# Kernel tuning notes

Hardware: AMD Instinct MI355X
Metric: run time of the kernel (lower is better)

Reference implementation:

```python
import jax, jax.numpy as jnp
import numpy as np

VOCAB, DIM, HEADS, LAYERS = 32000, 1024, 16, 2
B, S = 2, 1024
HD = DIM // HEADS


def rmsnorm(x, g, eps=1e-6):
    return x * jax.lax.rsqrt(jnp.mean(x * x, axis=-1, keepdims=True) + eps) * g


def setup_inputs() -> dict:
    key = jax.random.key(0)
    ks = jax.random.split(key, 20)
    s = 0.02
    d = {
        "text_ids": jax.random.randint(ks[0], (B, S), 0, VOCAB),
        "embed": jax.random.normal(ks[1], (VOCAB, DIM), jnp.float32) * s,
        "g1": jnp.ones((LAYERS, DIM), jnp.float32),
        "wq": jax.random.normal(ks[2], (LAYERS, DIM, DIM), jnp.float32) * s,
        "bq": jnp.zeros((LAYERS, DIM), jnp.float32),
        "wk": jax.random.normal(ks[3], (LAYERS, DIM, DIM), jnp.float32) * s,
        "bk": jnp.zeros((LAYERS, DIM), jnp.float32),
        "wv": jax.random.normal(ks[4], (LAYERS, DIM, DIM), jnp.float32) * s,
        "bv": jnp.zeros((LAYERS, DIM), jnp.float32),
        "wo": jax.random.normal(ks[5], (LAYERS, DIM, DIM), jnp.float32) * s,
        "bo": jnp.zeros((LAYERS, DIM), jnp.float32),
        "g2": jnp.ones((LAYERS, DIM), jnp.float32),
        "w1": jax.random.normal(ks[6], (LAYERS, DIM, 4 * DIM), jnp.float32) * s,
        "b1": jnp.zeros((LAYERS, 4 * DIM), jnp.float32),
        "w2": jax.random.normal(ks[7], (LAYERS, 4 * DIM, DIM), jnp.float32) * s,
        "b2": jnp.zeros((LAYERS, DIM), jnp.float32),
        "gf": jnp.ones((DIM,), jnp.float32),
        "head_w": jax.random.normal(ks[8], (DIM, VOCAB), jnp.float32) * s,
        "head_b": jnp.zeros((VOCAB,), jnp.float32),
    }
    return d


def reference(text_ids, embed, g1, wq, bq, wk, bk, wv, bv, wo, bo,
              g2, w1, b1, w2, b2, gf, head_w, head_b):
    b, s = text_ids.shape
    x = embed[text_ids]                                   # [B,S,D]
    causal = jnp.tril(jnp.ones((s, s), dtype=bool))        # [S,S]
    scale = 1.0 / jnp.sqrt(jnp.asarray(HD, x.dtype))
    for l in range(LAYERS):
        # attention sublayer: x = x + attn(norm1(x))
        h = rmsnorm(x, g1[l])
        q = (h @ wq[l] + bq[l]).reshape(b, s, HEADS, HD)
        k = (h @ wk[l] + bk[l]).reshape(b, s, HEADS, HD)
        v = (h @ wv[l] + bv[l]).reshape(b, s, HEADS, HD)
        scores = jnp.einsum("bqhd,bkhd->bhqk", q, k) * scale
        scores = jnp.where(causal, scores, jnp.asarray(-1e30, scores.dtype))
        a = jax.nn.softmax(scores, axis=-1)
        o = jnp.einsum("bhqk,bkhd->bqhd", a, v).reshape(b, s, DIM)
        x = x + (o @ wo[l] + bo[l])
        # FFN sublayer: x = x + ffn(norm2(x)), SiLU MLP (MoE unused in source forward)
        h2 = rmsnorm(x, g2[l])
        x = x + (jax.nn.silu(h2 @ w1[l] + b1[l]) @ w2[l] + b2[l])
    x = rmsnorm(x, gf)
    return x.astype(jnp.float32) @ head_w + head_b         # [B,S,VOCAB]
```

## Files before the change

### kernel.cpp

```cpp
#include <hip/hip_runtime.h>

#define LAYERS 2
#define DIM 1024
#define HEADS 16
#define HD 64
#define BATCH 2
#define SEQ 1024
#define ROWS (BATCH * SEQ)
#define FFN (4 * DIM)
#define VOCAB 32000
#define QKVN (3 * DIM)

typedef unsigned short u16;
typedef short vshort8 __attribute__((ext_vector_type(8)));
typedef float f32x4 __attribute__((ext_vector_type(4)));

#define VMCNT(n) asm volatile("s_waitcnt vmcnt(" #n ")" ::: "memory")

__device__ __forceinline__ u16 f2bf(float f) {
  union { float f; unsigned u; } x{f};
  unsigned r = (x.u + 0x7fffu + ((x.u >> 16) & 1u)) >> 16;
  return (u16)r;
}

__device__ __forceinline__ void gll16(const void* g, u16* l) {
  __builtin_amdgcn_global_load_lds(
      (const __attribute__((address_space(1))) void*)g,
      (__attribute__((address_space(3))) void*)l, 16, 0, 0);
}

__device__ __forceinline__ int xcd_swizzle(int orig, int nwg) {
  int q = nwg >> 3, r = nwg & 7;
  int xcd = orig & 7;
  int base = (xcd < r) ? xcd * (q + 1) : r * (q + 1) + (xcd - r) * q;
  return base + (orig >> 3);
}

__global__ __launch_bounds__(256) void transpose_f32_bf16(
    const float* __restrict__ src, u16* __restrict__ dst, int R, int C) {
  __shared__ float tile[32][33];
  int c0 = blockIdx.x * 32, r0 = blockIdx.y * 32;
  int tx = threadIdx.x, ty = threadIdx.y;
#pragma unroll
  for (int i = 0; i < 4; i++)
    tile[ty + i * 8][tx] = src[(size_t)(r0 + ty + i * 8) * C + c0 + tx];
  __syncthreads();
#pragma unroll
  for (int i = 0; i < 4; i++)
    dst[(size_t)(c0 + ty + i * 8) * R + r0 + tx] = f2bf(tile[tx][ty + i * 8]);
}

__global__ __launch_bounds__(256) void pack_qkv_bias(
    const float* __restrict__ bq, const float* __restrict__ bk,
    const float* __restrict__ bv, float* __restrict__ o) {
  int t = blockIdx.x * 256 + threadIdx.x;
  if (t < DIM) o[t] = bq[t];
  else if (t < 2 * DIM) o[t] = bk[t - DIM];
  else if (t < 3 * DIM) o[t] = bv[t - 2 * DIM];
}

__global__ __launch_bounds__(256) void embed_gather(
    const int* __restrict__ ids, const float* __restrict__ emb,
    float* __restrict__ x) {
  int row = blockIdx.x;
  int id = ids[row];
  const float4* s = (const float4*)(emb + (size_t)id * DIM);
  float4* d = (float4*)(x + (size_t)row * DIM);
  d[threadIdx.x] = s[threadIdx.x];
}

__global__ __launch_bounds__(256) void rmsnorm_kernel(
    const float* __restrict__ x, const float* __restrict__ g,
    u16* __restrict__ out) {
  int row = blockIdx.x;
  int t = threadIdx.x;
  const float4* xr = (const float4*)(x + (size_t)row * DIM);
  float4 v = xr[t];
  float ss = v.x * v.x + v.y * v.y + v.z * v.z + v.w * v.w;
  for (int off = 32; off > 0; off >>= 1) ss += __shfl_down(ss, off);
  __shared__ float part[4];
  if ((t & 63) == 0) part[t >> 6] = ss;
  __syncthreads();
  float tot = part[0] + part[1] + part[2] + part[3];
  float r = rsqrtf(tot / (float)DIM + 1e-6f);
  float4 gv = ((const float4*)g)[t];
  ushort4 o;
  o.x = f2bf(v.x * r * gv.x);
  o.y = f2bf(v.y * r * gv.y);
  o.z = f2bf(v.z * r * gv.z);
  o.w = f2bf(v.w * r * gv.w);
  *(ushort4*)(out + (size_t)row * DIM + t * 4) = o;
}

__global__ __launch_bounds__(256) void addnorm_kernel(
    float* __restrict__ x, const float* __restrict__ P0,
    const float* __restrict__ P1, const float* __restrict__ bias,
    const float* __restrict__ g, u16* __restrict__ h) {
  int row = blockIdx.x;
  int t = threadIdx.x;
  float4 v = ((const float4*)(x + (size_t)row * DIM))[t];
  float4 a = ((const float4*)(P0 + (size_t)row * DIM))[t];
  float4 b = ((const float4*)(P1 + (size_t)row * DIM))[t];
  float4 c = ((const float4*)bias)[t];
  v.x += a.x + b.x + c.x;
  v.y += a.y + b.y + c.y;
  v.z += a.z + b.z + c.z;
  v.w += a.w + b.w + c.w;
  ((float4*)(x + (size_t)row * DIM))[t] = v;
  float ss = v.x * v.x + v.y * v.y + v.z * v.z + v.w * v.w;
  for (int off = 32; off > 0; off >>= 1) ss += __shfl_down(ss, off);
  __shared__ float part[4];
  if ((t & 63) == 0) part[t >> 6] = ss;
  __syncthreads();
  float tot = part[0] + part[1] + part[2] + part[3];
  float r = rsqrtf(tot / (float)DIM + 1e-6f);
  float4 gv = ((const float4*)g)[t];
  ushort4 o;
  o.x = f2bf(v.x * r * gv.x);
  o.y = f2bf(v.y * r * gv.y);
  o.z = f2bf(v.z * r * gv.z);
  o.w = f2bf(v.w * r * gv.w);
  *(ushort4*)(h + (size_t)row * DIM + t * 4) = o;
}

template <int OUTBF, int SILU, int SPLITK, int MFAST>
__global__ __launch_bounds__(256, 2) void gemm128_kernel(
    const u16* __restrict__ A, const u16* __restrict__ Wt,
    const float* __restrict__ bias, void* __restrict__ outv,
    float* __restrict__ pout1, int M, int N, int K) {
  __shared__ u16 As[2][128 * 64];
  __shared__ u16 Bs[2][128 * 64];
  int nm = M >> 7, nn = N >> 7, nwg = nm * nn;
  int wg = xcd_swizzle(blockIdx.x, SPLITK ? nwg * 2 : nwg);
  int ks = 0;
  if (SPLITK) { ks = wg >= nwg; wg -= ks * nwg; }
  int mi, ni;
  if (MFAST) { mi = wg % nm; ni = wg / nm; }
  else       { ni = wg % nn; mi = wg / nn; }
  int m0 = mi << 7, n0 = ni << 7;
  int kb = SPLITK ? ks * (K >> 1) : 0;
  int NTt = (SPLITK ? (K >> 1) : K) >> 6;
  int tid = threadIdx.x, wave = tid >> 6, lane = tid & 63;
  int wr = wave >> 1, wc = wave & 1;
  int r16 = lane & 15, g4 = lane >> 4;
  int lrow = lane >> 3, lslot = lane & 7;

  f32x4 acc[4][4] = {};

  auto stage = [&](int buf, int kt) {
#pragma unroll
    for (int i = 0; i < 4; i++) {
      int s = wave * 4 + i;
      int row = s * 8 + lrow;
      int slot = lslot ^ (row & 7);
      gll16(A + (size_t)(m0 + row) * K + kb + kt * 64 + slot * 8,
            &As[buf][s * 512 + lane * 8]);
    }
#pragma unroll
    for (int i = 0; i < 4; i++) {
      int s = wave * 4 + i;
      int row = s * 8 + lrow;
      int slot = lslot ^ (row & 7);
      gll16(Wt + (size_t)(n0 + row) * K + kb + kt * 64 + slot * 8,
            &Bs[buf][s * 512 + lane * 8]);
    }
  };

  stage(0, 0);
  VMCNT(0);
  __builtin_amdgcn_s_barrier();

  for (int t = 0; t < NTt; t++) {
    int cur = t & 1;
    if (t + 1 < NTt) stage(cur ^ 1, t + 1);
#pragma unroll
    for (int kk = 0; kk < 2; kk++) {
      vshort8 af[4], bf[4];
#pragma unroll
      for (int m = 0; m < 4; m++) {
        int r = wr * 64 + m * 16 + r16;
        int slot = (kk * 4 + g4) ^ (r & 7);
        af[m] = *(const vshort8*)&As[cur][r * 64 + slot * 8];
      }
#pragma unroll
      for (int n = 0; n < 4; n++) {
        int c = wc * 64 + n * 16 + r16;
        int slot = (kk * 4 + g4) ^ (c & 7);
        bf[n] = *(const vshort8*)&Bs[cur][c * 64 + slot * 8];
      }
#pragma unroll
      for (int m = 0; m < 4; m++)
#pragma unroll
        for (int n = 0; n < 4; n++)
          acc[m][n] = __builtin_amdgcn_mfma_f32_16x16x32_bf16(af[m], bf[n],
                                                              acc[m][n], 0, 0, 0);
    }
    VMCNT(0);
    __builtin_amdgcn_s_barrier();
  }

  if (SPLITK) {
    float* P = ks ? pout1 : (float*)outv;
#pragma unroll
    for (int m = 0; m < 4; m++) {
      int rowb = m0 + wr * 64 + m * 16 + g4 * 4;
#pragma unroll
      for (int n = 0; n < 4; n++) {
        int col = n0 + wc * 64 + n * 16 + r16;
#pragma unroll
        for (int j = 0; j < 4; j++)
          P[(size_t)(rowb + j) * N + col] = acc[m][n][j];
      }
    }
  } else {
#pragma unroll
    for (int m = 0; m < 4; m++) {
      int rowb = m0 + wr * 64 + m * 16 + g4 * 4;
#pragma unroll
      for (int n = 0; n < 4; n++) {
        int col = n0 + wc * 64 + n * 16 + r16;
        float b = bias[col];
#pragma unroll
        for (int j = 0; j < 4; j++) {
          float v = acc[m][n][j] + b;
          if (SILU) v = v / (1.f + __expf(-v));
          if (OUTBF)
            ((u16*)outv)[(size_t)(rowb + j) * N + col] = f2bf(v);
          else
            ((float*)outv)[(size_t)(rowb + j) * N + col] = v;
        }
      }
    }
  }
}

__global__ __launch_bounds__(512, 2) void gemm256p_kernel(
    const u16* __restrict__ A, const u16* __restrict__ Wt,
    const float* __restrict__ bias, float* __restrict__ out,
    int M, int N, int K) {
  __shared__ u16 As[2][256 * 64];
  __shared__ u16 Bs[2][256 * 64];
  int nn = N >> 8;
  int wg = xcd_swizzle(blockIdx.x, nn * 2);
  int ni = wg >> 1, mhalf = wg & 1;
  int n0 = ni << 8;
  int tid = threadIdx.x, w = tid >> 6, lane = tid & 63;
  int wr = w >> 2, wc = w & 3;
  int r16 = lane & 15, g4 = lane >> 4;
  int srow8 = lane >> 3, sslot = lane & 7;
  const int NTK = 16;
  const int NGT = 64;

  f32x4 acc[8][4] = {};

  auto stageA = [&](int buf, int mb, int kt, int hb, int j) {
    int chunk = j * 8 + w;
    int row = hb * 128 + chunk * 8 + srow8;
    int slot = sslot ^ (row & 7);
    gll16(A + (size_t)(mb + row) * K + kt * 64 + slot * 8,
          &As[buf][hb * 8192 + chunk * 512 + lane * 8]);
  };
  auto stageB = [&](int buf, int kt, int hb, int j) {
    int chunk = j * 8 + w;
    int row = hb * 128 + chunk * 8 + srow8;
    int slot = sslot ^ (row & 7);
    gll16(Wt + (size_t)(n0 + row) * K + kt * 64 + slot * 8,
          &Bs[buf][hb * 8192 + chunk * 512 + lane * 8]);
  };
  auto readA = [&](int buf, int mf, int kk) -> vshort8 {
    int row = mf * 32 + wr * 16 + r16;
    int slot = (kk * 4 + g4) ^ (row & 7);
    return *(const vshort8*)&As[buf][row * 64 + slot * 8];
  };
  auto readB = [&](int buf, int nf, int kk) -> vshort8 {
    int row = nf * 64 + wc * 16 + r16;
    int slot = (kk * 4 + g4) ^ (row & 7);
    return *(const vshort8*)&Bs[buf][row * 64 + slot * 8];
  };

  int mb0 = (mhalf * 4) << 8;
  stageA(0, mb0, 0, 0, 0); stageA(0, mb0, 0, 0, 1);
  stageB(0, 0, 0, 0);      stageB(0, 0, 0, 1);
  stageB(0, 0, 1, 0);      stageB(0, 0, 1, 1);
  stageA(0, mb0, 0, 1, 0); stageA(0, mb0, 0, 1, 1);
  VMCNT(0);
  __builtin_amdgcn_s_barrier();

  vshort8 af[4][2], bf0[2][2], bf1[2][2];

  for (int ti = 0; ti < 4; ti++) {
    int m0 = (mhalf * 4 + ti) << 8;
    for (int tt = 0; tt < NTK; tt++) {
      int gt = ti * NTK + tt;
      int cur = gt & 1, nxt = cur ^ 1;
      int gt1 = gt + 1;
      bool hn = gt1 < NGT;
      int kt1 = gt1 & (NTK - 1);
      int mb1 = (mhalf * 4 + (gt1 >> 4)) << 8;
#pragma unroll
      for (int m = 0; m < 4; m++)
#pragma unroll
        for (int kk = 0; kk < 2; kk++) af[m][kk] = readA(cur, m, kk);
#pragma unroll
      for (int n = 0; n < 2; n++)
#pragma unroll
        for (int kk = 0; kk < 2; kk++) bf0[n][kk] = readB(cur, n, kk);
      if (hn) { stageA(nxt, mb1, kt1, 0, 0); stageA(nxt, mb1, kt1, 0, 1); }
      __builtin_amdgcn_s_barrier();
      __builtin_amdgcn_s_setprio(1);
#pragma unroll
      for (int m = 0; m < 4; m++)
#pragma unroll
        for (int n = 0; n < 2; n++)
#pragma unroll
          for (int kk = 0; kk < 2; kk++)
            acc[m][n] = __builtin_amdgcn_mfma_f32_16x16x32_bf16(
                af[m][kk], bf0[n][kk], acc[m][n], 0, 0, 0);
      __builtin_amdgcn_s_setprio(0);
      VMCNT(4);
      __builtin_amdgcn_s_barrier();
#pragma unroll
      for (int n = 0; n < 2; n++)
#pragma unroll
        for (int kk = 0; kk < 2; kk++) bf1[n][kk] = readB(cur, 2 + n, kk);
      if (hn) { stageB(nxt, kt1, 0, 0); stageB(nxt, kt1, 0, 1); }
      __builtin_amdgcn_s_barrier();
      __builtin_amdgcn_s_setprio(1);
#pragma unroll
      for (int m = 0; m < 4; m++)
#pragma unroll
        for (int n = 0; n < 2; n++)
#pragma unroll
          for (int kk = 0; kk < 2; kk++)
            acc[m][n + 2] = __builtin_amdgcn_mfma_f32_16x16x32_bf16(
                af[m][kk], bf1[n][kk], acc[m][n + 2], 0, 0, 0);
      __builtin_amdgcn_s_setprio(0);
      VMCNT(4);
      __builtin_amdgcn_s_barrier();
#pragma unroll
      for (int m = 0; m < 4; m++)
#pragma unroll
        for (int kk = 0; kk < 2; kk++) af[m][kk] = readA(cur, 4 + m, kk);
      if (hn) { stageB(nxt, kt1, 1, 0); stageB(nxt, kt1, 1, 1); }
      __builtin_amdgcn_s_barrier();
      __builtin_amdgcn_s_setprio(1);
#pragma unroll
      for (int m = 0; m < 4; m++)
#pragma unroll
        for (int n = 0; n < 2; n++)
#pragma unroll
          for (int kk = 0; kk < 2; kk++)
            acc[m + 4][n + 2] = __builtin_amdgcn_mfma_f32_16x16x32_bf16(
                af[m][kk], bf1[n][kk], acc[m + 4][n + 2], 0, 0, 0);
      __builtin_amdgcn_s_setprio(0);
      VMCNT(4);
      __builtin_amdgcn_s_barrier();
      if (hn) { stageA(nxt, mb1, kt1, 1, 0); stageA(nxt, mb1, kt1, 1, 1); }
      __builtin_amdgcn_s_barrier();
      __builtin_amdgcn_s_setprio(1);
#pragma unroll
      for (int m = 0; m < 4; m++)
#pragma unroll
        for (int n = 0; n < 2; n++)
#pragma unroll
          for (int kk = 0; kk < 2; kk++)
            acc[m + 4][n] = __builtin_amdgcn_mfma_f32_16x16x32_bf16(
                af[m][kk], bf0[n][kk], acc[m + 4][n], 0, 0, 0);
      __builtin_amdgcn_s_setprio(0);
      VMCNT(4);
      __builtin_amdgcn_s_barrier();
    }
#pragma unroll
    for (int mf = 0; mf < 8; mf++) {
      int rowb = m0 + mf * 32 + wr * 16 + g4 * 4;
#pragma unroll
      for (int nf = 0; nf < 4; nf++) {
        int col = n0 + nf * 64 + wc * 16 + r16;
        float b = bias[col];
#pragma unroll
        for (int j = 0; j < 4; j++)
          out[(size_t)(rowb + j) * N + col] = acc[mf][nf][j] + b;
      }
    }
#pragma unroll
    for (int mf = 0; mf < 8; mf++)
#pragma unroll
      for (int nf = 0; nf < 4; nf++) acc[mf][nf] = f32x4{0.f, 0.f, 0.f, 0.f};
  }
}

__global__ __launch_bounds__(256) void vtrans_kernel(const u16* __restrict__ qkv,
                                                     u16* __restrict__ vt2) {
  __shared__ u16 tl[64][80];
  int s0 = blockIdx.x * 64;
  int bh = blockIdx.y;
  int b = bh >> 4, h = bh & 15;
  int tid = threadIdx.x;
#pragma unroll
  for (int c = 0; c < 2; c++) {
    int idx = tid + c * 256;
    int row = idx >> 3;
    int col8 = (idx & 7) * 8;
    *(vshort8*)&tl[row][col8] = *(const vshort8*)
        &qkv[(size_t)(b * SEQ + s0 + row) * QKVN + 2 * DIM + h * HD + col8];
  }
  __syncthreads();
#pragma unroll
  for (int c = 0; c < 2; c++) {
    int idx = tid + c * 256;
    int s8l = idx >> 6;
    int d = idx & 63;
    vshort8 v;
#pragma unroll
    for (int j = 0; j < 8; j++) v[j] = (short)tl[s8l * 8 + j][d];
    *(vshort8*)&vt2[(((size_t)bh * (SEQ / 8) + (s0 >> 3) + s8l) * 64 + d) * 8] = v;
  }
}

__global__ __launch_bounds__(256) void attn_kernel(const u16* __restrict__ qkv,
                                                   const u16* __restrict__ vt2,
                                                   u16* __restrict__ o) {
  __shared__ u16 Ks[2][32 * 64];
  __shared__ u16 pl[4][16 * 40];
  int qblk = blockIdx.x, bh = blockIdx.y;
  int b = bh >> 4, h = bh & 15;
  int tid = threadIdx.x, w = tid >> 6, lane = tid & 63;
  int r16 = lane & 15, g4 = lane >> 4;
  int q0 = qblk * 64 + w * 16;

  const u16* qrow = qkv + ((size_t)(b * SEQ) + q0 + r16) * QKVN + h * HD;
  vshort8 aq0 = *(const vshort8*)(qrow + g4 * 8);
  vshort8 aq1 = *(const vshort8*)(qrow + 32 + g4 * 8);

  float mrun[4], lrun[4];
  f32x4 accO[4];
#pragma unroll
  for (int j = 0; j < 4; j++) { mrun[j] = -1e30f; lrun[j] = 0.f; }
#pragma unroll
  for (int d = 0; d < 4; d++) accO[d] = f32x4{0.f, 0.f, 0.f, 0.f};

  int nkvT = qblk * 2 + 2;
  auto stageK = [&](int buf, int kt) {
    int row = tid >> 3;
    int slot = (tid & 7) ^ (row & 7);
    gll16(qkv + ((size_t)(b * SEQ) + kt * 32 + row) * QKVN + DIM + h * HD + slot * 8,
          &Ks[buf][w * 512 + lane * 8]);
  };
  stageK(0, 0);
  __syncthreads();
  int buf = 0;
  for (int kt = 0; kt < nkvT; kt++) {
    int kv0 = kt * 32;
    if (kt + 1 < nkvT) stageK(buf ^ 1, kt + 1);
    if (kv0 <= q0 + 15) {
      int row0 = r16, row1 = 16 + r16;
      vshort8 bk00 = *(const vshort8*)&Ks[buf][row0 * 64 + ((0 + g4) ^ (row0 & 7)) * 8];
      vshort8 bk01 = *(const vshort8*)&Ks[buf][row0 * 64 + ((4 + g4) ^ (row0 & 7)) * 8];
      vshort8 bk10 = *(const vshort8*)&Ks[buf][row1 * 64 + ((0 + g4) ^ (row1 & 7)) * 8];
      vshort8 bk11 = *(const vshort8*)&Ks[buf][row1 * 64 + ((4 + g4) ^ (row1 & 7)) * 8];
      f32x4 s0 = {}, s1 = {};
      s0 = __builtin_amdgcn_mfma_f32_16x16x32_bf16(aq0, bk00, s0, 0, 0, 0);
      s0 = __builtin_amdgcn_mfma_f32_16x16x32_bf16(aq1, bk01, s0, 0, 0, 0);
      s1 = __builtin_amdgcn_mfma_f32_16x16x32_bf16(aq0, bk10, s1, 0, 0, 0);
      s1 = __builtin_amdgcn_mfma_f32_16x16x32_bf16(aq1, bk11, s1, 0, 0, 0);

#pragma unroll
      for (int j = 0; j < 4; j++) {
        int qg = q0 + g4 * 4 + j;
        float x0 = s0[j] * 0.125f;
        float x1 = s1[j] * 0.125f;
        if (kv0 + r16 > qg) x0 = -1e30f;
        if (kv0 + 16 + r16 > qg) x1 = -1e30f;
        float mx = fmaxf(x0, x1);
#pragma unroll
        for (int mm = 1; mm < 16; mm <<= 1) mx = fmaxf(mx, __shfl_xor(mx, mm));
        float mnew = fmaxf(mrun[j], mx);
        float alpha = __expf(mrun[j] - mnew);
        float p0 = __expf(x0 - mnew);
        float p1 = __expf(x1 - mnew);
        float rs = p0 + p1;
#pragma unroll
        for (int mm = 1; mm < 16; mm <<= 1) rs += __shfl_xor(rs, mm);
        lrun[j] = lrun[j] * alpha + rs;
        mrun[j] = mnew;
#pragma unroll
        for (int d = 0; d < 4; d++) accO[d][j] *= alpha;
        pl[w][(g4 * 4 + j) * 40 + r16] = f2bf(p0);
        pl[w][(g4 * 4 + j) * 40 + 16 + r16] = f2bf(p1);
      }
      asm volatile("s_waitcnt lgkmcnt(0)" ::: "memory");
      vshort8 ap = *(const vshort8*)&pl[w][r16 * 40 + g4 * 8];
      const u16* vbase = vt2 + (((size_t)bh * (SEQ / 8) + (kv0 >> 3) + g4) * 64) * 8;
#pragma unroll
      for (int d = 0; d < 4; d++) {
        vshort8 bv = *(const vshort8*)(vbase + (size_t)(d * 16 + r16) * 8);
        accO[d] = __builtin_amdgcn_mfma_f32_16x16x32_bf16(ap, bv, accO[d], 0, 0, 0);
      }
    }
    __syncthreads();
    buf ^= 1;
  }

#pragma unroll
  for (int j = 0; j < 4; j++) {
    float inv = 1.f / lrun[j];
    int row = q0 + g4 * 4 + j;
#pragma unroll
    for (int d = 0; d < 4; d++)
      o[((size_t)(b * SEQ) + row) * DIM + h * HD + d * 16 + r16] =
          f2bf(accO[d][j] * inv);
  }
}

extern "C" void kernel_launch(void* const* d_in, const int* in_sizes, int n_in,
                              void* d_out, int out_size, void* d_ws,
                              size_t ws_size, hipStream_t stream) {
  const int* ids = (const int*)d_in[0];
  const float* emb = (const float*)d_in[1];
  const float* g1 = (const float*)d_in[2];
  const float* wq = (const float*)d_in[3];
  const float* bq = (const float*)d_in[4];
  const float* wk = (const float*)d_in[5];
  const float* bk = (const float*)d_in[6];
  const float* wv = (const float*)d_in[7];
  const float* bv = (const float*)d_in[8];
  const float* wo = (const float*)d_in[9];
  const float* bo = (const float*)d_in[10];
  const float* g2 = (const float*)d_in[11];
  const float* w1 = (const float*)d_in[12];
  const float* b1 = (const float*)d_in[13];
  const float* w2 = (const float*)d_in[14];
  const float* b2 = (const float*)d_in[15];
  const float* gf = (const float*)d_in[16];
  const float* head_w = (const float*)d_in[17];
  const float* head_b = (const float*)d_in[18];
  float* out = (float*)d_out;

  char* ws = (char*)d_ws;
  size_t off = 0;
  auto alloc = [&](size_t bytes) -> char* {
    char* p = ws + off;
    off += (bytes + 255) & ~(size_t)255;
    return p;
  };
  u16* wqkvT = (u16*)alloc((size_t)LAYERS * QKVN * DIM * 2);
  u16* woT = (u16*)alloc((size_t)LAYERS * DIM * DIM * 2);
  u16* w1T = (u16*)alloc((size_t)LAYERS * DIM * FFN * 2);
  u16* w2T = (u16*)alloc((size_t)LAYERS * DIM * FFN * 2);
  u16* headT = (u16*)alloc((size_t)VOCAB * DIM * 2);
  float* bqkv = (float*)alloc((size_t)LAYERS * QKVN * 4);
  float* x = (float*)alloc((size_t)ROWS * DIM * 4);
  u16* h = (u16*)alloc((size_t)ROWS * DIM * 2);
  u16* qkvb = (u16*)alloc((size_t)ROWS * QKVN * 2);
  u16* vtb = (u16*)alloc((size_t)ROWS * DIM * 2);
  u16* ob = (u16*)alloc((size_t)ROWS * DIM * 2);
  u16* tb = (u16*)alloc((size_t)ROWS * FFN * 2);
  float* P0 = (float*)alloc((size_t)ROWS * DIM * 4);
  float* P1 = (float*)alloc((size_t)ROWS * DIM * 4);
  if (off > ws_size) return;

  dim3 tb32(32, 8);
  for (int l = 0; l < LAYERS; l++) {
    u16* base = wqkvT + (size_t)l * QKVN * DIM;
    transpose_f32_bf16<<<dim3(DIM / 32, DIM / 32), tb32, 0, stream>>>(
        wq + (size_t)l * DIM * DIM, base, DIM, DIM);
    transpose_f32_bf16<<<dim3(DIM / 32, DIM / 32), tb32, 0, stream>>>(
        wk + (size_t)l * DIM * DIM, base + (size_t)DIM * DIM, DIM, DIM);
    transpose_f32_bf16<<<dim3(DIM / 32, DIM / 32), tb32, 0, stream>>>(
        wv + (size_t)l * DIM * DIM, base + (size_t)2 * DIM * DIM, DIM, DIM);
    transpose_f32_bf16<<<dim3(DIM / 32, DIM / 32), tb32, 0, stream>>>(
        wo + (size_t)l * DIM * DIM, woT + (size_t)l * DIM * DIM, DIM, DIM);
    transpose_f32_bf16<<<dim3(FFN / 32, DIM / 32), tb32, 0, stream>>>(
        w1 + (size_t)l * DIM * FFN, w1T + (size_t)l * DIM * FFN, DIM, FFN);
    transpose_f32_bf16<<<dim3(DIM / 32, FFN / 32), tb32, 0, stream>>>(
        w2 + (size_t)l * DIM * FFN, w2T + (size_t)l * DIM * FFN, FFN, DIM);
    pack_qkv_bias<<<QKVN / 256, 256, 0, stream>>>(
        bq + (size_t)l * DIM, bk + (size_t)l * DIM, bv + (size_t)l * DIM,
        bqkv + (size_t)l * QKVN);
  }
  transpose_f32_bf16<<<dim3(VOCAB / 32, DIM / 32), tb32, 0, stream>>>(
      head_w, headT, DIM, VOCAB);

  embed_gather<<<ROWS, 256, 0, stream>>>(ids, emb, x);
  rmsnorm_kernel<<<ROWS, 256, 0, stream>>>(x, g1, h);

  for (int l = 0; l < LAYERS; l++) {
    gemm128_kernel<1, 0, 0, 1>
        <<<(ROWS / 128) * (QKVN / 128), 256, 0, stream>>>(
            h, wqkvT + (size_t)l * QKVN * DIM, bqkv + (size_t)l * QKVN,
            qkvb, nullptr, ROWS, QKVN, DIM);
    vtrans_kernel<<<dim3(SEQ / 64, BATCH * HEADS), 256, 0, stream>>>(qkvb, vtb);
    attn_kernel<<<dim3(SEQ / 64, BATCH * HEADS), 256, 0, stream>>>(qkvb, vtb, ob);
    gemm128_kernel<0, 0, 1, 0>
        <<<2 * (ROWS / 128) * (DIM / 128), 256, 0, stream>>>(
            ob, woT + (size_t)l * DIM * DIM, nullptr, P0, P1, ROWS, DIM, DIM);
    addnorm_kernel<<<ROWS, 256, 0, stream>>>(
        x, P0, P1, bo + (size_t)l * DIM, g2 + (size_t)l * DIM, h);
    gemm128_kernel<1, 1, 0, 1>
        <<<(ROWS / 128) * (FFN / 128), 256, 0, stream>>>(
            h, w1T + (size_t)l * DIM * FFN, b1 + (size_t)l * FFN, tb, nullptr,
            ROWS, FFN, DIM);
    gemm128_kernel<0, 0, 1, 0>
        <<<2 * (ROWS / 128) * (DIM / 128), 256, 0, stream>>>(
            tb, w2T + (size_t)l * DIM * FFN, nullptr, P0, P1, ROWS, DIM, FFN);
    addnorm_kernel<<<ROWS, 256, 0, stream>>>(
        x, P0, P1, b2 + (size_t)l * DIM,
        (l == LAYERS - 1) ? gf : (g1 + (size_t)(l + 1) * DIM), h);
  }
  gemm256p_kernel<<<(VOCAB / 256) * 2, 512, 0, stream>>>(
      h, headT, head_b, out, ROWS, VOCAB, DIM);
}
```

Before: 634.2 us.

## Batch weight transposes, fuse V transpose into QKV GEMM, restructure LM-head pipeline

The per-layer weight transpose and bias-pack launches are merged into a few batched kernels indexed by blockIdx.z or y, which cuts launch count. The separate vtrans kernel is removed: the QKV GEMM epilogue writes the V columns straight into the transposed layout that attention expects. The LM-head GEMM main loop is rescheduled to issue all next-tile loads up front, fuse the B-fragment reads, and halve the barrier phases per k-step, with adjusted vmcnt waits. These changes risk stalls from altered wait counts and from strided 8-byte V stores.

```diff
diff --git a/kernel.cpp b/kernel.cpp
--- a/kernel.cpp
+++ b/kernel.cpp
@@ -36,9 +36,36 @@
   return base + (orig >> 3);
 }
 
-__global__ __launch_bounds__(256) void transpose_f32_bf16(
-    const float* __restrict__ src, u16* __restrict__ dst, int R, int C) {
+__global__ __launch_bounds__(256) void transpose_sq_kernel(
+    const float* __restrict__ wq, const float* __restrict__ wk,
+    const float* __restrict__ wv, const float* __restrict__ wo,
+    u16* __restrict__ wqkvT, u16* __restrict__ woT) {
   __shared__ float tile[32][33];
+  int z = blockIdx.z, l = z >> 2, wsel = z & 3;
+  const float* src =
+      (wsel == 0 ? wq : wsel == 1 ? wk : wsel == 2 ? wv : wo) +
+      (size_t)l * DIM * DIM;
+  u16* dst = (wsel < 3)
+                 ? wqkvT + (size_t)l * QKVN * DIM + (size_t)wsel * DIM * DIM
+                 : woT + (size_t)l * DIM * DIM;
+  int c0 = blockIdx.x * 32, r0 = blockIdx.y * 32;
+  int tx = threadIdx.x, ty = threadIdx.y;
+#pragma unroll
+  for (int i = 0; i < 4; i++)
+    tile[ty + i * 8][tx] = src[(size_t)(r0 + ty + i * 8) * DIM + c0 + tx];
+  __syncthreads();
+#pragma unroll
+  for (int i = 0; i < 4; i++)
+    dst[(size_t)(c0 + ty + i * 8) * DIM + r0 + tx] = f2bf(tile[tx][ty + i * 8]);
+}
+
+template <int R, int C>
+__global__ __launch_bounds__(256) void transpose_rc_kernel(
+    const float* __restrict__ srcb, u16* __restrict__ dstb) {
+  __shared__ float tile[32][33];
+  int l = blockIdx.z;
+  const float* src = srcb + (size_t)l * R * C;
+  u16* dst = dstb + (size_t)l * R * C;
   int c0 = blockIdx.x * 32, r0 = blockIdx.y * 32;
   int tx = threadIdx.x, ty = threadIdx.y;
 #pragma unroll
@@ -53,10 +80,13 @@
 __global__ __launch_bounds__(256) void pack_qkv_bias(
     const float* __restrict__ bq, const float* __restrict__ bk,
     const float* __restrict__ bv, float* __restrict__ o) {
+  int l = blockIdx.y;
   int t = blockIdx.x * 256 + threadIdx.x;
-  if (t < DIM) o[t] = bq[t];
-  else if (t < 2 * DIM) o[t] = bk[t - DIM];
-  else if (t < 3 * DIM) o[t] = bv[t - 2 * DIM];
+  float v;
+  if (t < DIM) v = bq[l * DIM + t];
+  else if (t < 2 * DIM) v = bk[l * DIM + t - DIM];
+  else v = bv[l * DIM + t - 2 * DIM];
+  o[(size_t)l * QKVN + t] = v;
 }
 
 __global__ __launch_bounds__(256) void embed_gather(
@@ -123,11 +153,11 @@
   *(ushort4*)(h + (size_t)row * DIM + t * 4) = o;
 }
 
-template <int OUTBF, int SILU, int SPLITK, int MFAST>
+template <int OUTBF, int SILU, int SPLITK, int MFAST, int VT>
 __global__ __launch_bounds__(256, 2) void gemm128_kernel(
     const u16* __restrict__ A, const u16* __restrict__ Wt,
     const float* __restrict__ bias, void* __restrict__ outv,
-    float* __restrict__ pout1, int M, int N, int K) {
+    float* __restrict__ pout1, u16* __restrict__ vt2, int M, int N, int K) {
   __shared__ u16 As[2][128 * 64];
   __shared__ u16 Bs[2][128 * 64];
   int nm = M >> 7, nn = N >> 7, nwg = nm * nn;
@@ -220,14 +250,27 @@
       for (int n = 0; n < 4; n++) {
         int col = n0 + wc * 64 + n * 16 + r16;
         float b = bias[col];
+        u16 ov[4];
 #pragma unroll
         for (int j = 0; j < 4; j++) {
           float v = acc[m][n][j] + b;
           if (SILU) v = v / (1.f + __expf(-v));
-          if (OUTBF)
-            ((u16*)outv)[(size_t)(rowb + j) * N + col] = f2bf(v);
-          else
-            ((float*)outv)[(size_t)(rowb + j) * N + col] = v;
+          if (OUTBF) ov[j] = f2bf(v);
+          else ((float*)outv)[(size_t)(rowb + j) * N + col] = v;
+        }
+        if (OUTBF) {
+          if (VT && col >= 2 * DIM) {
+            int dv = col - 2 * DIM;
+            int hh = dv >> 6, dd = dv & 63;
+            int bb = rowb >> 10, s = rowb & 1023;
+            ushort4 o4{ov[0], ov[1], ov[2], ov[3]};
+            *(ushort4*)&vt2[((((size_t)(bb * 16 + hh) * (SEQ / 8) + (s >> 3)) * 64 +
+                              dd) * 8) + (s & 7)] = o4;
+          } else {
+#pragma unroll
+            for (int j = 0; j < 4; j++)
+              ((u16*)outv)[(size_t)(rowb + j) * N + col] = ov[j];
+          }
         }
       }
     }
@@ -283,7 +326,7 @@
   stageB(0, 0, 0, 0);      stageB(0, 0, 0, 1);
   stageB(0, 0, 1, 0);      stageB(0, 0, 1, 1);
   stageA(0, mb0, 0, 1, 0); stageA(0, mb0, 0, 1, 1);
-  VMCNT(0);
+  VMCNT(2);
   __builtin_amdgcn_s_barrier();
 
   vshort8 af[4][2], bf0[2][2], bf1[2][2];
@@ -297,6 +340,11 @@
       bool hn = gt1 < NGT;
       int kt1 = gt1 & (NTK - 1);
       int mb1 = (mhalf * 4 + (gt1 >> 4)) << 8;
+      if (hn) {
+        stageA(nxt, mb1, kt1, 0, 0); stageA(nxt, mb1, kt1, 0, 1);
+        stageB(nxt, kt1, 0, 0);      stageB(nxt, kt1, 0, 1);
+        stageB(nxt, kt1, 1, 0);      stageB(nxt, kt1, 1, 1);
+      }
 #pragma unroll
       for (int m = 0; m < 4; m++)
 #pragma unroll
@@ -304,8 +352,10 @@
 #pragma unroll
       for (int n = 0; n < 2; n++)
 #pragma unroll
-        for (int kk = 0; kk < 2; kk++) bf0[n][kk] = readB(cur, n, kk);
-      if (hn) { stageA(nxt, mb1, kt1, 0, 0); stageA(nxt, mb1, kt1, 0, 1); }
+        for (int kk = 0; kk < 2; kk++) {
+          bf0[n][kk] = readB(cur, n, kk);
+          bf1[n][kk] = readB(cur, 2 + n, kk);
+        }
       __builtin_amdgcn_s_barrier();
       __builtin_amdgcn_s_setprio(1);
 #pragma unroll
@@ -313,17 +363,20 @@
 #pragma unroll
         for (int n = 0; n < 2; n++)
 #pragma unroll
-          for (int kk = 0; kk < 2; kk++)
+          for (int kk = 0; kk < 2; kk++) {
             acc[m][n] = __builtin_amdgcn_mfma_f32_16x16x32_bf16(
                 af[m][kk], bf0[n][kk], acc[m][n], 0, 0, 0);
+            acc[m][n + 2] = __builtin_amdgcn_mfma_f32_16x16x32_bf16(
+                af[m][kk], bf1[n][kk], acc[m][n + 2], 0, 0, 0);
+          }
       __builtin_amdgcn_s_setprio(0);
-      VMCNT(4);
+      VMCNT(6);
       __builtin_amdgcn_s_barrier();
-#pragma unroll
-      for (int n = 0; n < 2; n++)
-#pragma unroll
-        for (int kk = 0; kk < 2; kk++) bf1[n][kk] = readB(cur, 2 + n, kk);
-      if (hn) { stageB(nxt, kt1, 0, 0); stageB(nxt, kt1, 0, 1); }
+      if (hn) { stageA(nxt, mb1, kt1, 1, 0); stageA(nxt, mb1, kt1, 1, 1); }
+#pragma unroll
+      for (int m = 0; m < 4; m++)
+#pragma unroll
+        for (int kk = 0; kk < 2; kk++) af[m][kk] = readA(cur, 4 + m, kk);
       __builtin_amdgcn_s_barrier();
       __builtin_amdgcn_s_setprio(1);
 #pragma unroll
@@ -331,43 +384,14 @@
 #pragma unroll
         for (int n = 0; n < 2; n++)
 #pragma unroll
-          for (int kk = 0; kk < 2; kk++)
-            acc[m][n + 2] = __builtin_amdgcn_mfma_f32_16x16x32_bf16(
-                af[m][kk], bf1[n][kk], acc[m][n + 2], 0, 0, 0);
-      __builtin_amdgcn_s_setprio(0);
-      VMCNT(4);
-      __builtin_amdgcn_s_barrier();
-#pragma unroll
-      for (int m = 0; m < 4; m++)
-#pragma unroll
-        for (int kk = 0; kk < 2; kk++) af[m][kk] = readA(cur, 4 + m, kk);
-      if (hn) { stageB(nxt, kt1, 1, 0); stageB(nxt, kt1, 1, 1); }
-      __builtin_amdgcn_s_barrier();
-      __builtin_amdgcn_s_setprio(1);
-#pragma unroll
-      for (int m = 0; m < 4; m++)
-#pragma unroll
-        for (int n = 0; n < 2; n++)
-#pragma unroll
-          for (int kk = 0; kk < 2; kk++)
+          for (int kk = 0; kk < 2; kk++) {
+            acc[m + 4][n] = __builtin_amdgcn_mfma_f32_16x16x32_bf16(
+                af[m][kk], bf0[n][kk], acc[m + 4][n], 0, 0, 0);
             acc[m + 4][n + 2] = __builtin_amdgcn_mfma_f32_16x16x32_bf16(
                 af[m][kk], bf1[n][kk], acc[m + 4][n + 2], 0, 0, 0);
+          }
       __builtin_amdgcn_s_setprio(0);
-      VMCNT(4);
-      __builtin_amdgcn_s_barrier();
-      if (hn) { stageA(nxt, mb1, kt1, 1, 0); stageA(nxt, mb1, kt1, 1, 1); }
-      __builtin_amdgcn_s_barrier();
-      __builtin_amdgcn_s_setprio(1);
-#pragma unroll
-      for (int m = 0; m < 4; m++)
-#pragma unroll
-        for (int n = 0; n < 2; n++)
-#pragma unroll
-          for (int kk = 0; kk < 2; kk++)
-            acc[m + 4][n] = __builtin_amdgcn_mfma_f32_16x16x32_bf16(
-                af[m][kk], bf0[n][kk], acc[m + 4][n], 0, 0, 0);
-      __builtin_amdgcn_s_setprio(0);
-      VMCNT(4);
+      VMCNT(2);
       __builtin_amdgcn_s_barrier();
     }
 #pragma unroll
@@ -386,34 +410,6 @@
     for (int mf = 0; mf < 8; mf++)
 #pragma unroll
       for (int nf = 0; nf < 4; nf++) acc[mf][nf] = f32x4{0.f, 0.f, 0.f, 0.f};
-  }
-}
-
-__global__ __launch_bounds__(256) void vtrans_kernel(const u16* __restrict__ qkv,
-                                                     u16* __restrict__ vt2) {
-  __shared__ u16 tl[64][80];
-  int s0 = blockIdx.x * 64;
-  int bh = blockIdx.y;
-  int b = bh >> 4, h = bh & 15;
-  int tid = threadIdx.x;
-#pragma unroll
-  for (int c = 0; c < 2; c++) {
-    int idx = tid + c * 256;
-    int row = idx >> 3;
-    int col8 = (idx & 7) * 8;
-    *(vshort8*)&tl[row][col8] = *(const vshort8*)
-        &qkv[(size_t)(b * SEQ + s0 + row) * QKVN + 2 * DIM + h * HD + col8];
-  }
-  __syncthreads();
-#pragma unroll
-  for (int c = 0; c < 2; c++) {
-    int idx = tid + c * 256;
-    int s8l = idx >> 6;
-    int d = idx & 63;
-    vshort8 v;
-#pragma unroll
-    for (int j = 0; j < 8; j++) v[j] = (short)tl[s8l * 8 + j][d];
-    *(vshort8*)&vt2[(((size_t)bh * (SEQ / 8) + (s0 >> 3) + s8l) * 64 + d) * 8] = v;
   }
 }
 
@@ -560,49 +556,39 @@
   if (off > ws_size) return;
 
   dim3 tb32(32, 8);
-  for (int l = 0; l < LAYERS; l++) {
-    u16* base = wqkvT + (size_t)l * QKVN * DIM;
-    transpose_f32_bf16<<<dim3(DIM / 32, DIM / 32), tb32, 0, stream>>>(
-        wq + (size_t)l * DIM * DIM, base, DIM, DIM);
-    transpose_f32_bf16<<<dim3(DIM / 32, DIM / 32), tb32, 0, stream>>>(
-        wk + (size_t)l * DIM * DIM, base + (size_t)DIM * DIM, DIM, DIM);
-    transpose_f32_bf16<<<dim3(DIM / 32, DIM / 32), tb32, 0, stream>>>(
-        wv + (size_t)l * DIM * DIM, base + (size_t)2 * DIM * DIM, DIM, DIM);
-    transpose_f32_bf16<<<dim3(DIM / 32, DIM / 32), tb32, 0, stream>>>(
-        wo + (size_t)l * DIM * DIM, woT + (size_t)l * DIM * DIM, DIM, DIM);
-    transpose_f32_bf16<<<dim3(FFN / 32, DIM / 32), tb32, 0, stream>>>(
-        w1 + (size_t)l * DIM * FFN, w1T + (size_t)l * DIM * FFN, DIM, FFN);
-    transpose_f32_bf16<<<dim3(DIM / 32, FFN / 32), tb32, 0, stream>>>(
-        w2 + (size_t)l * DIM * FFN, w2T + (size_t)l * DIM * FFN, FFN, DIM);
-    pack_qkv_bias<<<QKVN / 256, 256, 0, stream>>>(
-        bq + (size_t)l * DIM, bk + (size_t)l * DIM, bv + (size_t)l * DIM,
-        bqkv + (size_t)l * QKVN);
-  }
-  transpose_f32_bf16<<<dim3(VOCAB / 32, DIM / 32), tb32, 0, stream>>>(
-      head_w, headT, DIM, VOCAB);
+  transpose_sq_kernel<<<dim3(DIM / 32, DIM / 32, 4 * LAYERS), tb32, 0, stream>>>(
+      wq, wk, wv, wo, wqkvT, woT);
+  transpose_rc_kernel<DIM, FFN>
+      <<<dim3(FFN / 32, DIM / 32, LAYERS), tb32, 0, stream>>>(w1, w1T);
+  transpose_rc_kernel<FFN, DIM>
+      <<<dim3(DIM / 32, FFN / 32, LAYERS), tb32, 0, stream>>>(w2, w2T);
+  transpose_rc_kernel<DIM, VOCAB>
+      <<<dim3(VOCAB / 32, DIM / 32, 1), tb32, 0, stream>>>(head_w, headT);
+  pack_qkv_bias<<<dim3(QKVN / 256, LAYERS), 256, 0, stream>>>(bq, bk, bv, bqkv);
 
   embed_gather<<<ROWS, 256, 0, stream>>>(ids, emb, x);
   rmsnorm_kernel<<<ROWS, 256, 0, stream>>>(x, g1, h);
 
   for (int l = 0; l < LAYERS; l++) {
-    gemm128_kernel<1, 0, 0, 1>
+    gemm128_kernel<1, 0, 0, 1, 1>
         <<<(ROWS / 128) * (QKVN / 128), 256, 0, stream>>>(
             h, wqkvT + (size_t)l * QKVN * DIM, bqkv + (size_t)l * QKVN,
-            qkvb, nullptr, ROWS, QKVN, DIM);
-    vtrans_kernel<<<dim3(SEQ / 64, BATCH * HEADS), 256, 0, stream>>>(qkvb, vtb);
+            qkvb, nullptr, vtb, ROWS, QKVN, DIM);
     attn_kernel<<<dim3(SEQ / 64, BATCH * HEADS), 256, 0, stream>>>(qkvb, vtb, ob);
-    gemm128_kernel<0, 0, 1, 0>
+    gemm128_kernel<0, 0, 1, 0, 0>
         <<<2 * (ROWS / 128) * (DIM / 128), 256, 0, stream>>>(
-            ob, woT + (size_t)l * DIM * DIM, nullptr, P0, P1, ROWS, DIM, DIM);
+            ob, woT + (size_t)l * DIM * DIM, nullptr, P0, P1, nullptr,
+            ROWS, DIM, DIM);
     addnorm_kernel<<<ROWS, 256, 0, stream>>>(
         x, P0, P1, bo + (size_t)l * DIM, g2 + (size_t)l * DIM, h);
-    gemm128_kernel<1, 1, 0, 1>
+    gemm128_kernel<1, 1, 0, 1, 0>
         <<<(ROWS / 128) * (FFN / 128), 256, 0, stream>>>(
             h, w1T + (size_t)l * DIM * FFN, b1 + (size_t)l * FFN, tb, nullptr,
-            ROWS, FFN, DIM);
-    gemm128_kernel<0, 0, 1, 0>
+            nullptr, ROWS, FFN, DIM);
+    gemm128_kernel<0, 0, 1, 0, 0>
         <<<2 * (ROWS / 128) * (DIM / 128), 256, 0, stream>>>(
-            tb, w2T + (size_t)l * DIM * FFN, nullptr, P0, P1, ROWS, DIM, FFN);
+            tb, w2T + (size_t)l * DIM * FFN, nullptr, P0, P1, nullptr,
+            ROWS, DIM, FFN);
     addnorm_kernel<<<ROWS, 256, 0, stream>>>(
         x, P0, P1, b2 + (size_t)l * DIM,
         (l == LAYERS - 1) ? gf : (g1 + (size_t)(l + 1) * DIM), h);
```

After: 658.4 us. 1.04x slower.
